# Kernel optimization log

Hardware: AMD Instinct MI355X
Metric: run time of the kernel (lower is better)

The kernel has to match this reference:

```python
import jax, jax.numpy as jnp
import numpy as np
import math

D_MODEL = 512
N_HEADS = 8
D_K = 64
BS = 16
SEQ = 512


def setup_inputs() -> dict:
    key = jax.random.key(0)
    ks = jax.random.split(key, 15)
    f = lambda k, sh, s=1.0: jax.random.normal(k, sh, dtype=jnp.float32) * s
    inp = {}
    for i, n in enumerate(["q_mean", "q_cov", "k_mean", "k_cov", "v_mean", "v_cov"]):
        inp[n] = f(ks[i], (BS, SEQ, D_MODEL))
    wscale = 1.0 / math.sqrt(D_MODEL)  # ~xavier
    for i, n in enumerate(["Wq_mean", "Wq_cov", "Wk_mean", "Wk_cov", "Wv_mean", "Wv_cov", "Wo_mean", "Wo_cov"]):
        inp[n] = f(ks[6 + i], (D_MODEL, D_MODEL), wscale)
    inp["gammas"] = f(ks[14], (N_HEADS, 1, 1), 0.5)  # xavier on (h,1,1)
    # causal mask: attend to positions j <= i
    inp["mask"] = jnp.tril(jnp.ones((SEQ, SEQ), dtype=jnp.int32))[None, None]
    return inp


def _heads(x, W):
    # torch Linear: x @ W.T ; bias is 0 by init. -> [bs, h, S, d_k]
    bs = x.shape[0]
    return (x @ W.T).reshape(bs, -1, N_HEADS, D_K).transpose(0, 2, 1, 3)


def _uattention(qm, qc, km, kc, vm, vc, mask, gammas):
    # Wasserstein-2 distance between diagonal Gaussians, fused into matmuls
    mean_d = (-2.0 * jnp.einsum('bhsd,bhtd->bhst', qm, km)
              + jnp.sum(qm ** 2, -1, keepdims=True)
              + jnp.sum(km ** 2, -1, keepdims=True).swapaxes(-1, -2))
    sqc = jnp.sqrt(jnp.clip(qc, 1e-24))
    skc = jnp.sqrt(jnp.clip(kc, 1e-24))
    cov_d = (-2.0 * jnp.einsum('bhsd,bhtd->bhst', sqc, skc)
             + jnp.sum(qc, -1, keepdims=True)
             + jnp.sum(kc, -1, keepdims=True).swapaxes(-1, -2))
    scores = -(mean_d + cov_d) / math.sqrt(D_K)  # [bs,h,S,S]

    maskb = (mask == 0)
    maskf = mask.astype(scores.dtype)

    def _dist(s):
        s_ = jax.nn.softmax(jnp.where(maskb, -1e32, s), axis=-1) * maskf
        cum = jnp.cumsum(s_, axis=-1)
        tot = jnp.sum(s_, axis=-1, keepdims=True)
        idx = jnp.arange(SEQ)
        pos = jnp.abs(idx[None, :] - idx[:, None]).astype(jnp.float32)[None, None]
        return jnp.sqrt(jnp.clip((tot - cum) * pos, 0.0))

    dist_scores = jax.lax.stop_gradient(_dist(scores))  # torch: no_grad + detach
    gamma = -jax.nn.softplus(gammas)[None]  # [1,h,1,1]
    total_effect = jnp.clip(jnp.exp(dist_scores * gamma), 1e-5, 1e5)
    scores = jnp.where(maskb, -1e32, scores * total_effect)
    scores = jax.nn.softmax(scores, axis=-1)
    scores = scores.at[:, :, 0, :].set(0.0)  # zero_pad
    out_mean = jnp.einsum('bhst,bhtd->bhsd', scores, vm)
    out_cov = jnp.einsum('bhst,bhtd->bhsd', scores ** 2, vc)
    return out_mean, out_cov


def reference(q_mean, q_cov, k_mean, k_cov, v_mean, v_cov,
              Wq_mean, Wq_cov, Wk_mean, Wk_cov, Wv_mean, Wv_cov,
              Wo_mean, Wo_cov, gammas, mask):
    bs = q_mean.shape[0]
    qm = _heads(q_mean, Wq_mean)
    qc = _heads(q_cov, Wq_cov)
    km = _heads(k_mean, Wk_mean)
    kc = _heads(k_cov, Wk_cov)
    vm = _heads(v_mean, Wv_mean)
    vc = _heads(v_cov, Wv_cov)
    om, oc = _uattention(qm, qc, km, kc, vm, vc, mask, gammas)
    cm = om.transpose(0, 2, 1, 3).reshape(bs, -1, D_MODEL)
    cc = oc.transpose(0, 2, 1, 3).reshape(bs, -1, D_MODEL)
    return cm @ Wo_mean.T, cc @ Wo_cov.T
```

## Files before the change

### kernel.cpp

```cpp
#include <hip/hip_runtime.h>
#include <hip/hip_bf16.h>

#define SEQ    512
#define DMODEL 512
#define NHEAD  8
#define DK     64
#define BS     16
#define NBH    (BS*NHEAD)
#define HSZ    (SEQ*DK)

typedef __attribute__((ext_vector_type(8))) short bf16x8;
typedef __attribute__((ext_vector_type(4))) float f32x4;

#define MFMA32(A,B,C) __builtin_amdgcn_mfma_f32_16x16x32_bf16(A,B,C,0,0,0)

#define WS_GAM 16ull
#define WS_AQM 256ull
#define WS_AQC (WS_AQM +  65536ull)
#define WS_BKM (WS_AQM + 131072ull)
#define WS_BKC (WS_AQM + 196608ull)
#define WS_AQF (WS_AQM + 262144ull)
#define WS_BKF (WS_AQM + 327680ull)
#define WS_OM  1048576ull
#define WS_OC  (WS_OM + 4194304ull)
#define WS_BF  (WS_OC + 4194304ull)
#define ARRE   4194304ull
#define A_QMH 0
#define A_QML 1
#define A_SCH 2
#define A_SCL 3
#define A_KMH 4
#define A_SKH 6
#define A_VMT 8
#define A_VCT 9

__device__ __forceinline__ unsigned short* warr(float* wsf, int idx) {
  return (unsigned short*)(wsf + WS_BF) + (size_t)idx * ARRE;
}

__device__ __forceinline__ float bf2f(unsigned short h) {
  union { float f; unsigned u; } v; v.u = ((unsigned)h) << 16; return v.f;
}
__device__ __forceinline__ unsigned short f2bf(float f) {
  union { float f; unsigned u; } v; v.f = f;
  unsigned u = v.u;
  u += 0x7FFFu + ((u >> 16) & 1u);
  return (unsigned short)(u >> 16);
}
__device__ __forceinline__ void ld8_f32(const float* p, float* v) {
  float4 a = *(const float4*)p; float4 b = *(const float4*)(p+4);
  v[0]=a.x;v[1]=a.y;v[2]=a.z;v[3]=a.w;v[4]=b.x;v[5]=b.y;v[6]=b.z;v[7]=b.w;
}
__device__ __forceinline__ unsigned pk2bf(float a, float b) {
  union { float f; unsigned u; } x, y;
  x.f = a; y.f = b;
  return __builtin_amdgcn_perm(y.u + 0x8000u, x.u + 0x8000u, 0x07060302u);
}
__device__ __forceinline__ uint4 cvt8r(const float* t8) {
  uint4 h;
  h.x = pk2bf(t8[0], t8[1]);
  h.y = pk2bf(t8[2], t8[3]);
  h.z = pk2bf(t8[4], t8[5]);
  h.w = pk2bf(t8[6], t8[7]);
  return h;
}
__device__ __forceinline__ uint4 cvt8h(const float* p) {
  float t8[8]; ld8_f32(p, t8); return cvt8r(t8);
}

__global__ void k_gamma(const float* __restrict__ g_in, float* __restrict__ wsf) {
  int t = threadIdx.x;
  if (t >= NHEAD) return;
  float g = g_in[t];
  float sp = (g > 20.f) ? g : log1pf(expf(g));
  (wsf + WS_GAM)[t] = -sp;
}

__global__ __launch_bounds__(256) void k_projM(
    const float* xqm, const float* xqc, const float* xkm, const float* xkc,
    const float* xvm, const float* xvc,
    const float* wqm, const float* wqc, const float* wkm, const float* wkc,
    const float* wvm, const float* wvc,
    float* wsf)
{
  __shared__ __align__(16) unsigned short Ah[4096];
  __shared__ __align__(16) unsigned short Bh[4096];
  const int y = blockIdx.y;
  const float* X; const float* W;
  unsigned short *outh = nullptr, *outl = nullptr;
  float* sums = nullptr;
  float qscale = 1.0f; int mode = 0;
  switch (y) {
    case 0: X=xqm; W=wqm; outh=warr(wsf,A_QMH); outl=warr(wsf,A_QML); sums=wsf+WS_AQM; qscale=0.25f; mode=0; break;
    case 1: X=xkm; W=wkm; outh=warr(wsf,A_KMH); outl=nullptr;         sums=wsf+WS_BKM; qscale=1.0f;  mode=0; break;
    case 2: X=xqc; W=wqc; outh=warr(wsf,A_SCH); outl=warr(wsf,A_SCL); sums=wsf+WS_AQC; qscale=0.25f; mode=1; break;
    case 3: X=xkc; W=wkc; outh=warr(wsf,A_SKH); outl=nullptr;         sums=wsf+WS_BKC; qscale=1.0f;  mode=1; break;
    case 4: X=xvm; W=wvm; outh=warr(wsf,A_VMT); mode=2; break;
    default:X=xvc; W=wvc; outh=warr(wsf,A_VCT); mode=2; break;
  }
  const int tid = threadIdx.x;
  const int l = tid & 63, li = l & 15, lg = l >> 4;
  const int w = tid >> 6, wr = w >> 1, wc = w & 1;
  const int blk = blockIdx.x;
  const int xcd = blk & 7, qq = blk >> 3;
  const int m0 = (xcd*8 + (qq & 7)) * 128;
  const int n0 = (qq >> 3) * 128;
  const int r0 = tid >> 2, c0 = tid & 3, r1 = r0 + 64;
  const int wo0 = r0*64 + ((c0 ^ ((r0>>1)&3))*16);
  const int wo1 = r1*64 + ((c0 ^ ((r1>>1)&3))*16);
  int roA[4], roB[4];
#pragma unroll
  for (int mi = 0; mi < 4; ++mi) {
    int r  = wr*64 + mi*16 + li;
    roA[mi] = r*64 + ((lg ^ ((r>>1)&3))*16);
    int rn = wc*64 + mi*16 + li;
    roB[mi] = rn*64 + ((lg ^ ((rn>>1)&3))*16);
  }
  const float* xp0 = X + (size_t)(m0+r0)*DMODEL + c0*8;
  const float* xp1 = X + (size_t)(m0+r1)*DMODEL + c0*8;
  const float* wp0 = W + (size_t)(n0+r0)*DMODEL + c0*8;
  const float* wp1 = W + (size_t)(n0+r1)*DMODEL + c0*8;
  uint4 a0 = cvt8h(xp0);
  uint4 a1 = cvt8h(xp1);
  uint4 b0 = cvt8h(wp0);
  uint4 b1 = cvt8h(wp1);

  f32x4 acc[4][4];
  f32x4 z = {0.f,0.f,0.f,0.f};
#pragma unroll
  for (int a = 0; a < 4; ++a)
#pragma unroll
    for (int b = 0; b < 4; ++b) acc[a][b] = z;

  for (int kt = 0; kt < DMODEL; kt += 32) {
    __syncthreads();
    *(uint4*)((char*)Ah + wo0) = a0;
    *(uint4*)((char*)Ah + wo1) = a1;
    *(uint4*)((char*)Bh + wo0) = b0;
    *(uint4*)((char*)Bh + wo1) = b1;
    __syncthreads();
    if (kt + 32 < DMODEL) {
      a0 = cvt8h(xp0 + kt + 32);
      a1 = cvt8h(xp1 + kt + 32);
      b0 = cvt8h(wp0 + kt + 32);
      b1 = cvt8h(wp1 + kt + 32);
    }
    bf16x8 ah[4], bh[4];
#pragma unroll
    for (int mi = 0; mi < 4; ++mi) {
      ah[mi] = *(const bf16x8*)((const char*)Ah + roA[mi]);
      bh[mi] = *(const bf16x8*)((const char*)Bh + roB[mi]);
    }
#pragma unroll
    for (int mi = 0; mi < 4; ++mi)
#pragma unroll
      for (int nj = 0; nj < 4; ++nj)
        acc[mi][nj] = MFMA32(ah[mi], bh[nj], acc[mi][nj]);
  }

  const int head = ((n0 >> 6) + wc);
  if (mode <= 1) {
    const bool kside = (outl == nullptr);
#pragma unroll
    for (int mi = 0; mi < 4; ++mi)
#pragma unroll
      for (int reg = 0; reg < 4; ++reg) {
        float rs = 0.f;
#pragma unroll
        for (int nj = 0; nj < 4; ++nj) {
          float v = acc[mi][nj][reg];
          if (mode == 0) {
            float vs = (kside) ? bf2f(f2bf(v)) : v;
            rs += vs*vs;
          } else {
            rs += v;
          }
        }
        rs += __shfl_xor(rs, 1); rs += __shfl_xor(rs, 2);
        rs += __shfl_xor(rs, 4); rs += __shfl_xor(rs, 8);
        if (li == 0) {
          int m = m0 + wr*64 + mi*16 + 4*lg + reg;
          sums[((size_t)(m >> 9)*NHEAD + head)*SEQ + (m & 511)] = rs;
        }
      }
#pragma unroll
    for (int mi = 0; mi < 4; ++mi)
#pragma unroll
      for (int nj = 0; nj < 4; ++nj)
#pragma unroll
        for (int reg = 0; reg < 4; ++reg) {
          float v = acc[mi][nj][reg];
          if (mode == 1) v = sqrtf(fmaxf(v, 1e-24f));
          v *= qscale;
          unsigned short h16 = f2bf(v);
          int m = m0 + wr*64 + mi*16 + 4*lg + reg;
          int n = n0 + wc*64 + nj*16 + li;
          size_t dst = ((size_t)((m >> 9)*NHEAD + (n >> 6))*SEQ + (m & 511))*DK + (n & 63);
          outh[dst] = h16;
          if (outl) outl[dst] = f2bf(v - bf2f(h16));
        }
  } else {
#pragma unroll
    for (int mi = 0; mi < 4; ++mi)
#pragma unroll
      for (int nj = 0; nj < 4; ++nj) {
        int mb = m0 + wr*64 + mi*16 + 4*lg;
        int n = n0 + wc*64 + nj*16 + li;
        int b = mb >> 9, s = mb & 511, d = n & 63;
        unsigned e0 = f2bf(acc[mi][nj][0]);
        unsigned e1 = f2bf(acc[mi][nj][1]);
        unsigned e2 = f2bf(acc[mi][nj][2]);
        unsigned e3 = f2bf(acc[mi][nj][3]);
        uint2 pk; pk.x = e0 | (e1 << 16); pk.y = e2 | (e3 << 16);
        *(uint2*)(outh + ((size_t)(b*NHEAD + head)*DK + d)*SEQ + s) = pk;
      }
  }
}

__global__ void k_sumAB(float* wsf) {
  int i = blockIdx.x * 256 + threadIdx.x;
  if (i < NBH*SEQ) {
    (wsf+WS_AQF)[i] = 0.125f * ((wsf+WS_AQM)[i] + (wsf+WS_AQC)[i]);
    (wsf+WS_BKF)[i] = 0.125f * ((wsf+WS_BKM)[i] + (wsf+WS_BKC)[i]);
  }
}

__global__ __launch_bounds__(128) void k_attn2(float* wsf)
{
  __shared__ float s_bk[SEQ];
  __shared__ float s_ex[2][2][16];
  __shared__ __align__(16) float s_acc[64][33];

  const unsigned short* qmh = warr(wsf, A_QMH);
  const unsigned short* qml = warr(wsf, A_QML);
  const unsigned short* sch = warr(wsf, A_SCH);
  const unsigned short* scl = warr(wsf, A_SCL);
  const unsigned short* kmh = warr(wsf, A_KMH);
  const unsigned short* skh = warr(wsf, A_SKH);
  const unsigned short* vmT = warr(wsf, A_VMT);
  const unsigned short* vcT = warr(wsf, A_VCT);
  float* omF = wsf + WS_OM;
  float* ocF = wsf + WS_OC;
  const float* AqF = wsf + WS_AQF;
  const float* BkF = wsf + WS_BKF;

  const int tid = threadIdx.x;
  const int l = tid & 63, li = l & 15, lg = l >> 4;
  const int w = tid >> 6;
  const int blk = blockIdx.x;
  const int xcd = blk & 7;
  const int q   = blk >> 3;
  const int bh  = xcd*16 + (q & 15);
  const int rt  = 31 - (q >> 4);
  const int i = rt*16 + li;
  const int ntile = rt + 1;
  const int h0 = (ntile + 1) >> 1;
  const int tstart = w ? h0 : 0;
  const int tend   = w ? ntile : h0;
  const float gam = (wsf + WS_GAM)[bh & (NHEAD-1)];
  const float aq = AqF[(size_t)bh*SEQ + i];

  for (int idx = tid; idx < SEQ; idx += 128) s_bk[idx] = BkF[(size_t)bh*SEQ + idx];

  bf16x8 qf[8];
  {
    const unsigned short* qb[4] = {qmh, qml, sch, scl};
#pragma unroll
    for (int part = 0; part < 2; ++part)
#pragma unroll
      for (int hl = 0; hl < 2; ++hl)
#pragma unroll
        for (int ks = 0; ks < 2; ++ks)
          qf[part*4 + ks*2 + hl] =
            *(const bf16x8*)(qb[part*2+hl] + ((size_t)bh*SEQ + i)*DK + ks*32 + lg*8);
  }
  __syncthreads();

  auto score_tile = [&](int t, float* s) {
    const int j0 = t*16;
    f32x4 accA = {0.f,0.f,0.f,0.f};
    f32x4 accB = {0.f,0.f,0.f,0.f};
    const size_t krow = ((size_t)bh*SEQ + j0 + li)*DK + lg*8;
#pragma unroll
    for (int part = 0; part < 2; ++part) {
      const unsigned short* khp = part ? skh : kmh;
#pragma unroll
      for (int ks = 0; ks < 2; ++ks) {
        bf16x8 kh = *(const bf16x8*)(khp + krow + ks*32);
        accA = MFMA32(kh, qf[part*4+ks*2+0], accA);
        accB = MFMA32(kh, qf[part*4+ks*2+1], accB);
      }
    }
    const float4 bk4 = *(const float4*)&s_bk[j0 + lg*4];
    float bks[4] = {bk4.x, bk4.y, bk4.z, bk4.w};
#pragma unroll
    for (int r = 0; r < 4; ++r) {
      int j = j0 + lg*4 + r;
      float v = (accA[r] + accB[r]) - aq - bks[r];
      s[r] = (j > i) ? -3.0e38f : v;
    }
  };

  float m1 = -3.0e38f, tot = 0.f;
  for (int t = tstart; t < tend; ++t) {
    float s[4]; score_tile(t, s);
    float tm = fmaxf(fmaxf(s[0], s[1]), fmaxf(s[2], s[3]));
    tm = fmaxf(tm, __shfl_xor(tm, 16));
    tm = fmaxf(tm, __shfl_xor(tm, 32));
    float m1n = fmaxf(m1, tm);
    float lsum = __expf(s[0]-m1n) + __expf(s[1]-m1n) + __expf(s[2]-m1n) + __expf(s[3]-m1n);
    lsum += __shfl_xor(lsum, 16); lsum += __shfl_xor(lsum, 32);
    tot = tot * __expf(m1 - m1n) + lsum;
    m1 = m1n;
  }
  if (lg == 0) { s_ex[w][0][li] = m1; s_ex[w][1][li] = tot; }
  __syncthreads();
  float run;
  {
    float m0 = s_ex[0][0][li], t0 = s_ex[0][1][li];
    float m1b = s_ex[1][0][li], t1 = s_ex[1][1][li];
    float mg = fmaxf(m0, m1b);
    float e0 = __expf(m0 - mg), e1 = __expf(m1b - mg);
    tot = t0*e0 + t1*e1;
    run = w ? t0*e0 : 0.f;
    m1 = mg;
  }
  const float invtot = 1.0f / tot;

  f32x4 accm[4], accc[4];
  {
    f32x4 z = {0.f,0.f,0.f,0.f};
#pragma unroll
    for (int dt = 0; dt < 4; ++dt) { accm[dt] = z; accc[dt] = z; }
  }
  float m2 = -3.0e38f, sum2 = 0.f;

  auto scan_tile = [&](int t, float* s2) {
    float s[4]; score_tile(t, s);
    float e0 = __expf(s[0]-m1), e1 = __expf(s[1]-m1),
          e2 = __expf(s[2]-m1), e3 = __expf(s[3]-m1);
    float p0 = e0, p1 = p0+e1, p2 = p1+e2, p3 = p2+e3;
    float lt = p3;
    float a = __shfl_up(lt, 16), b = __shfl_up(lt, 32), c = __shfl_up(lt, 48);
    float excl = (lg >= 1 ? a : 0.f) + (lg >= 2 ? b : 0.f) + (lg >= 3 ? c : 0.f);
    float base = run + excl;
    float cums[4] = {base+p0, base+p1, base+p2, base+p3};
    float ttr = lt;
    ttr += __shfl_xor(ttr, 16); ttr += __shfl_xor(ttr, 32);
    run += ttr;
#pragma unroll
    for (int r = 0; r < 4; ++r) {
      int j = t*16 + lg*4 + r;
      float rem = fmaxf(tot - cums[r], 0.f) * invtot;
      float pos = fmaxf((float)(i - j), 0.f);
      float dist = sqrtf(rem * pos);
      float eff = fmaxf(__expf(dist * gam), 1e-5f);
      s2[r] = (j > i) ? -3.0e38f : s[r] * eff;
    }
  };

  for (int t0 = tstart; t0 < tend; t0 += 2) {
    float s2A[4], s2B[4];
    scan_tile(t0, s2A);
    const bool hasB = (t0 + 1) < tend;
    if (hasB) scan_tile(t0+1, s2B);
    else { s2B[0]=s2B[1]=s2B[2]=s2B[3] = -3.0e38f; }
    float mt = fmaxf(fmaxf(fmaxf(s2A[0],s2A[1]), fmaxf(s2A[2],s2A[3])),
                     fmaxf(fmaxf(s2B[0],s2B[1]), fmaxf(s2B[2],s2B[3])));
    mt = fmaxf(mt, __shfl_xor(mt, 16));
    mt = fmaxf(mt, __shfl_xor(mt, 32));
    float m2n = fmaxf(m2, mt);
    float scale = __expf(m2 - m2n);
    float scale2 = scale * scale;
#pragma unroll
    for (int dt = 0; dt < 4; ++dt) { accm[dt] *= scale; accc[dt] *= scale2; }
    float pA[4], pB[4];
#pragma unroll
    for (int r = 0; r < 4; ++r) { pA[r] = __expf(s2A[r]-m2n); pB[r] = __expf(s2B[r]-m2n); }
    float ps = pA[0]+pA[1]+pA[2]+pA[3] + pB[0]+pB[1]+pB[2]+pB[3];
    ps += __shfl_xor(ps, 16); ps += __shfl_xor(ps, 32);
    sum2 = sum2 * scale + ps;
    m2 = m2n;
    union PU { uint4 u; bf16x8 v; } pm, pc;
    pm.u.x = pk2bf(pA[0], pA[1]); pm.u.y = pk2bf(pA[2], pA[3]);
    pm.u.z = pk2bf(pB[0], pB[1]); pm.u.w = pk2bf(pB[2], pB[3]);
    pc.u.x = pk2bf(pA[0]*pA[0], pA[1]*pA[1]); pc.u.y = pk2bf(pA[2]*pA[2], pA[3]*pA[3]);
    pc.u.z = pk2bf(pB[0]*pB[0], pB[1]*pB[1]); pc.u.w = pk2bf(pB[2]*pB[2], pB[3]*pB[3]);
    const int j0A = t0*16;
    const int j0B = hasB ? j0A + 16 : j0A;
    union V16 { struct { uint2 lo, hi; } u; bf16x8 v; };
#pragma unroll
    for (int dt = 0; dt < 4; ++dt) {
      const size_t vrow = ((size_t)bh*DK + dt*16 + li)*SEQ;
      V16 vm_, vc_;
      vm_.u.lo = *(const uint2*)(vmT + vrow + j0A + lg*4);
      vm_.u.hi = *(const uint2*)(vmT + vrow + j0B + lg*4);
      vc_.u.lo = *(const uint2*)(vcT + vrow + j0A + lg*4);
      vc_.u.hi = *(const uint2*)(vcT + vrow + j0B + lg*4);
      accm[dt] = MFMA32(vm_.v, pm.v, accm[dt]);
      accc[dt] = MFMA32(vc_.v, pc.v, accc[dt]);
    }
  }

  __syncthreads();
  if (lg == 0) s_ex[w][0][li] = m2;
  __syncthreads();
  const float m2g = fmaxf(s_ex[0][0][li], s_ex[1][0][li]);
  const float sc = __expf(m2 - m2g);
  const float sc2 = sc * sc;
  if (w == 1) {
#pragma unroll
    for (int dt = 0; dt < 4; ++dt)
#pragma unroll
      for (int reg = 0; reg < 4; ++reg) {
        s_acc[l][dt*4 + reg]      = accm[dt][reg] * sc;
        s_acc[l][16 + dt*4 + reg] = accc[dt][reg] * sc2;
      }
    if (lg == 0) s_ex[1][1][li] = sum2 * sc;
  }
  __syncthreads();
  if (w == 0) {
    const float sum2g = sum2 * sc + s_ex[1][1][li];
    const float inv2 = 1.0f / sum2g;
    const float inv2c = inv2 * inv2;
    const bool zero = (i == 0);
    float* om_p = omF + ((size_t)bh*SEQ + i)*DK;
    float* oc_p = ocF + ((size_t)bh*SEQ + i)*DK;
#pragma unroll
    for (int dt = 0; dt < 4; ++dt) {
      float4 vm4, vc4;
      vm4.x = (accm[dt][0]*sc + s_acc[l][dt*4+0]) * inv2;
      vm4.y = (accm[dt][1]*sc + s_acc[l][dt*4+1]) * inv2;
      vm4.z = (accm[dt][2]*sc + s_acc[l][dt*4+2]) * inv2;
      vm4.w = (accm[dt][3]*sc + s_acc[l][dt*4+3]) * inv2;
      vc4.x = (accc[dt][0]*sc2 + s_acc[l][16+dt*4+0]) * inv2c;
      vc4.y = (accc[dt][1]*sc2 + s_acc[l][16+dt*4+1]) * inv2c;
      vc4.z = (accc[dt][2]*sc2 + s_acc[l][16+dt*4+2]) * inv2c;
      vc4.w = (accc[dt][3]*sc2 + s_acc[l][16+dt*4+3]) * inv2c;
      if (zero) { vm4 = make_float4(0.f,0.f,0.f,0.f); vc4 = vm4; }
      *(float4*)(om_p + dt*16 + lg*4) = vm4;
      *(float4*)(oc_p + dt*16 + lg*4) = vc4;
    }
  }
}

__global__ __launch_bounds__(256) void k_outM(float* wsf,
                                              const float* w_mean, const float* w_cov,
                                              float* outp)
{
  __shared__ __align__(16) unsigned short Ah[4096];
  __shared__ __align__(16) unsigned short Bh[4096];
  const int y = blockIdx.y;
  const float* A = wsf + (y ? WS_OC : WS_OM);
  const float* W = y ? w_cov : w_mean;
  float* out = outp + (size_t)y * 4194304ull;

  const int tid = threadIdx.x;
  const int l = tid & 63, li = l & 15, lg = l >> 4;
  const int w = tid >> 6, wr = w >> 1, wc = w & 1;
  const int blk = blockIdx.x;
  const int xcd = blk & 7, qq = blk >> 3;
  const int m0 = (xcd*8 + (qq & 7)) * 128;
  const int n0 = (qq >> 3) * 128;
  const int r0 = tid >> 2, c0 = tid & 3, r1 = r0 + 64;
  const int wo0 = r0*64 + ((c0 ^ ((r0>>1)&3))*16);
  const int wo1 = r1*64 + ((c0 ^ ((r1>>1)&3))*16);
  int roA[4], roB[4];
#pragma unroll
  for (int mi = 0; mi < 4; ++mi) {
    int r  = wr*64 + mi*16 + li;
    roA[mi] = r*64 + ((lg ^ ((r>>1)&3))*16);
    int rn = wc*64 + mi*16 + li;
    roB[mi] = rn*64 + ((lg ^ ((rn>>1)&3))*16);
  }
  const int mA0 = m0 + r0, mA1 = m0 + r1;
  const size_t abase0 = ((size_t)(mA0 >> 9) * NHEAD * SEQ + (mA0 & 511)) * DK;
  const size_t abase1 = ((size_t)(mA1 >> 9) * NHEAD * SEQ + (mA1 & 511)) * DK;
  const float* wp0 = W + (size_t)(n0 + r0)*DMODEL + c0*8;
  const float* wp1 = W + (size_t)(n0 + r1)*DMODEL + c0*8;

  auto acvt = [&](size_t abase, int k) -> uint4 {
    const float* p = A + abase + (size_t)(k >> 6) * (SEQ*DK) + (k & 63);
    return cvt8h(p);
  };

  int k0 = c0*8;
  uint4 a0 = acvt(abase0, k0);
  uint4 a1 = acvt(abase1, k0);
  uint4 b0 = cvt8h(wp0);
  uint4 b1 = cvt8h(wp1);

  f32x4 acc[4][4];
  f32x4 z = {0.f,0.f,0.f,0.f};
#pragma unroll
  for (int a = 0; a < 4; ++a)
#pragma unroll
    for (int b = 0; b < 4; ++b) acc[a][b] = z;

  for (int kt = 0; kt < DMODEL; kt += 32) {
    __syncthreads();
    *(uint4*)((char*)Ah + wo0) = a0;
    *(uint4*)((char*)Ah + wo1) = a1;
    *(uint4*)((char*)Bh + wo0) = b0;
    *(uint4*)((char*)Bh + wo1) = b1;
    __syncthreads();
    if (kt + 32 < DMODEL) {
      int kn = kt + 32 + c0*8;
      a0 = acvt(abase0, kn);
      a1 = acvt(abase1, kn);
      b0 = cvt8h(wp0 + kt + 32);
      b1 = cvt8h(wp1 + kt + 32);
    }
    bf16x8 ah[4], bh[4];
#pragma unroll
    for (int mi = 0; mi < 4; ++mi) {
      ah[mi] = *(const bf16x8*)((const char*)Ah + roA[mi]);
      bh[mi] = *(const bf16x8*)((const char*)Bh + roB[mi]);
    }
#pragma unroll
    for (int mi = 0; mi < 4; ++mi)
#pragma unroll
      for (int nj = 0; nj < 4; ++nj)
        acc[mi][nj] = MFMA32(ah[mi], bh[nj], acc[mi][nj]);
  }
#pragma unroll
  for (int mi = 0; mi < 4; ++mi)
#pragma unroll
    for (int nj = 0; nj < 4; ++nj)
#pragma unroll
      for (int reg = 0; reg < 4; ++reg) {
        int m = m0 + wr*64 + mi*16 + 4*lg + reg;
        int n = n0 + wc*64 + nj*16 + li;
        out[(size_t)m*DMODEL + n] = acc[mi][nj][reg];
      }
}

extern "C" void kernel_launch(void* const* d_in, const int* in_sizes, int n_in,
                              void* d_out, int out_size, void* d_ws, size_t ws_size,
                              hipStream_t stream) {
  (void)in_sizes; (void)n_in; (void)out_size; (void)ws_size;
  float* wsf = (float*)d_ws;

  k_gamma<<<1, 64, 0, stream>>>((const float*)d_in[14], wsf);
  k_projM<<<dim3(256, 6), 256, 0, stream>>>(
      (const float*)d_in[0], (const float*)d_in[1],
      (const float*)d_in[2], (const float*)d_in[3],
      (const float*)d_in[4], (const float*)d_in[5],
      (const float*)d_in[6], (const float*)d_in[7],
      (const float*)d_in[8], (const float*)d_in[9],
      (const float*)d_in[10], (const float*)d_in[11],
      wsf);
  k_sumAB<<<256, 256, 0, stream>>>(wsf);
  k_attn2<<<4096, 128, 0, stream>>>(wsf);
  k_outM<<<dim3(256, 2), 256, 0, stream>>>(wsf, (const float*)d_in[12],
                                           (const float*)d_in[13], (float*)d_out);
}
```

Measured before the change: 243.6 us.

## Split attention key range across four waves and use exp2 with prescaled scores

Each attention block now uses four waves instead of two. Each wave takes a quarter of the causal key tiles, and the partial softmax statistics and accumulators are merged through shared memory. Scores and gamma are prescaled by log2(e) so exp2 can replace expf, and the V tile loads are hoisted ahead of the softmax math to hide latency. This shortens the per-block serial chain at the cost of more shared memory, an extra merge step, and higher register pressure.

```diff
diff --git a/kernel.cpp b/kernel.cpp
--- a/kernel.cpp
+++ b/kernel.cpp
@@ -8,6 +8,7 @@
 #define BS     16
 #define NBH    (BS*NHEAD)
 #define HSZ    (SEQ*DK)
+#define L2E    1.4426950408889634f
 
 typedef __attribute__((ext_vector_type(8))) short bf16x8;
 typedef __attribute__((ext_vector_type(4))) float f32x4;
@@ -73,7 +74,7 @@
   if (t >= NHEAD) return;
   float g = g_in[t];
   float sp = (g > 20.f) ? g : log1pf(expf(g));
-  (wsf + WS_GAM)[t] = -sp;
+  (wsf + WS_GAM)[t] = -sp * L2E;
 }
 
 __global__ __launch_bounds__(256) void k_projM(
@@ -91,10 +92,10 @@
   float* sums = nullptr;
   float qscale = 1.0f; int mode = 0;
   switch (y) {
-    case 0: X=xqm; W=wqm; outh=warr(wsf,A_QMH); outl=warr(wsf,A_QML); sums=wsf+WS_AQM; qscale=0.25f; mode=0; break;
-    case 1: X=xkm; W=wkm; outh=warr(wsf,A_KMH); outl=nullptr;         sums=wsf+WS_BKM; qscale=1.0f;  mode=0; break;
-    case 2: X=xqc; W=wqc; outh=warr(wsf,A_SCH); outl=warr(wsf,A_SCL); sums=wsf+WS_AQC; qscale=0.25f; mode=1; break;
-    case 3: X=xkc; W=wkc; outh=warr(wsf,A_SKH); outl=nullptr;         sums=wsf+WS_BKC; qscale=1.0f;  mode=1; break;
+    case 0: X=xqm; W=wqm; outh=warr(wsf,A_QMH); outl=warr(wsf,A_QML); sums=wsf+WS_AQM; qscale=0.25f*L2E; mode=0; break;
+    case 1: X=xkm; W=wkm; outh=warr(wsf,A_KMH); outl=nullptr;         sums=wsf+WS_BKM; qscale=1.0f;      mode=0; break;
+    case 2: X=xqc; W=wqc; outh=warr(wsf,A_SCH); outl=warr(wsf,A_SCL); sums=wsf+WS_AQC; qscale=0.25f*L2E; mode=1; break;
+    case 3: X=xkc; W=wkc; outh=warr(wsf,A_SKH); outl=nullptr;         sums=wsf+WS_BKC; qscale=1.0f;      mode=1; break;
     case 4: X=xvm; W=wvm; outh=warr(wsf,A_VMT); mode=2; break;
     default:X=xvc; W=wvc; outh=warr(wsf,A_VCT); mode=2; break;
   }
@@ -220,16 +221,16 @@
 __global__ void k_sumAB(float* wsf) {
   int i = blockIdx.x * 256 + threadIdx.x;
   if (i < NBH*SEQ) {
-    (wsf+WS_AQF)[i] = 0.125f * ((wsf+WS_AQM)[i] + (wsf+WS_AQC)[i]);
-    (wsf+WS_BKF)[i] = 0.125f * ((wsf+WS_BKM)[i] + (wsf+WS_BKC)[i]);
-  }
-}
-
-__global__ __launch_bounds__(128) void k_attn2(float* wsf)
+    (wsf+WS_AQF)[i] = (0.125f*L2E) * ((wsf+WS_AQM)[i] + (wsf+WS_AQC)[i]);
+    (wsf+WS_BKF)[i] = (0.125f*L2E) * ((wsf+WS_BKM)[i] + (wsf+WS_BKC)[i]);
+  }
+}
+
+__global__ __launch_bounds__(256) void k_attn2(float* wsf)
 {
   __shared__ float s_bk[SEQ];
-  __shared__ float s_ex[2][2][16];
-  __shared__ __align__(16) float s_acc[64][33];
+  __shared__ float s_ex[4][2][16];
+  __shared__ __align__(16) float s_acc[3][64][33];
 
   const unsigned short* qmh = warr(wsf, A_QMH);
   const unsigned short* qml = warr(wsf, A_QML);
@@ -254,13 +255,13 @@
   const int rt  = 31 - (q >> 4);
   const int i = rt*16 + li;
   const int ntile = rt + 1;
-  const int h0 = (ntile + 1) >> 1;
-  const int tstart = w ? h0 : 0;
-  const int tend   = w ? ntile : h0;
+  const int qd = ntile >> 2, rr = ntile & 3;
+  const int tstart = w*qd + (w < rr ? w : rr);
+  const int tend   = tstart + qd + (w < rr ? 1 : 0);
   const float gam = (wsf + WS_GAM)[bh & (NHEAD-1)];
   const float aq = AqF[(size_t)bh*SEQ + i];
 
-  for (int idx = tid; idx < SEQ; idx += 128) s_bk[idx] = BkF[(size_t)bh*SEQ + idx];
+  for (int idx = tid; idx < SEQ; idx += 256) s_bk[idx] = BkF[(size_t)bh*SEQ + idx];
 
   bf16x8 qf[8];
   {
@@ -308,21 +309,24 @@
     tm = fmaxf(tm, __shfl_xor(tm, 16));
     tm = fmaxf(tm, __shfl_xor(tm, 32));
     float m1n = fmaxf(m1, tm);
-    float lsum = __expf(s[0]-m1n) + __expf(s[1]-m1n) + __expf(s[2]-m1n) + __expf(s[3]-m1n);
+    float lsum = exp2f(s[0]-m1n) + exp2f(s[1]-m1n) + exp2f(s[2]-m1n) + exp2f(s[3]-m1n);
     lsum += __shfl_xor(lsum, 16); lsum += __shfl_xor(lsum, 32);
-    tot = tot * __expf(m1 - m1n) + lsum;
+    tot = tot * exp2f(m1 - m1n) + lsum;
     m1 = m1n;
   }
   if (lg == 0) { s_ex[w][0][li] = m1; s_ex[w][1][li] = tot; }
   __syncthreads();
   float run;
   {
-    float m0 = s_ex[0][0][li], t0 = s_ex[0][1][li];
-    float m1b = s_ex[1][0][li], t1 = s_ex[1][1][li];
-    float mg = fmaxf(m0, m1b);
-    float e0 = __expf(m0 - mg), e1 = __expf(m1b - mg);
-    tot = t0*e0 + t1*e1;
-    run = w ? t0*e0 : 0.f;
+    float mA = s_ex[0][0][li], mB = s_ex[1][0][li],
+          mC = s_ex[2][0][li], mD = s_ex[3][0][li];
+    float mg = fmaxf(fmaxf(mA, mB), fmaxf(mC, mD));
+    float tA = s_ex[0][1][li] * exp2f(mA - mg);
+    float tB = s_ex[1][1][li] * exp2f(mB - mg);
+    float tC = s_ex[2][1][li] * exp2f(mC - mg);
+    float tD = s_ex[3][1][li] * exp2f(mD - mg);
+    tot = tA + tB + tC + tD;
+    run = (w > 0 ? tA : 0.f) + (w > 1 ? tB : 0.f) + (w > 2 ? tC : 0.f);
     m1 = mg;
   }
   const float invtot = 1.0f / tot;
@@ -337,8 +341,8 @@
 
   auto scan_tile = [&](int t, float* s2) {
     float s[4]; score_tile(t, s);
-    float e0 = __expf(s[0]-m1), e1 = __expf(s[1]-m1),
-          e2 = __expf(s[2]-m1), e3 = __expf(s[3]-m1);
+    float e0 = exp2f(s[0]-m1), e1 = exp2f(s[1]-m1),
+          e2 = exp2f(s[2]-m1), e3 = exp2f(s[3]-m1);
     float p0 = e0, p1 = p0+e1, p2 = p1+e2, p3 = p2+e3;
     float lt = p3;
     float a = __shfl_up(lt, 16), b = __shfl_up(lt, 32), c = __shfl_up(lt, 48);
@@ -354,7 +358,7 @@
       float rem = fmaxf(tot - cums[r], 0.f) * invtot;
       float pos = fmaxf((float)(i - j), 0.f);
       float dist = sqrtf(rem * pos);
-      float eff = fmaxf(__expf(dist * gam), 1e-5f);
+      float eff = fmaxf(exp2f(dist * gam), 1e-5f);
       s2[r] = (j > i) ? -3.0e38f : s[r] * eff;
     }
   };
@@ -365,18 +369,30 @@
     const bool hasB = (t0 + 1) < tend;
     if (hasB) scan_tile(t0+1, s2B);
     else { s2B[0]=s2B[1]=s2B[2]=s2B[3] = -3.0e38f; }
+    const int j0A = t0*16;
+    const int j0B = hasB ? j0A + 16 : j0A;
+    union V16 { struct { uint2 lo, hi; } u; bf16x8 v; };
+    V16 vm_[4], vc_[4];
+#pragma unroll
+    for (int dt = 0; dt < 4; ++dt) {
+      const size_t vrow = ((size_t)bh*DK + dt*16 + li)*SEQ;
+      vm_[dt].u.lo = *(const uint2*)(vmT + vrow + j0A + lg*4);
+      vm_[dt].u.hi = *(const uint2*)(vmT + vrow + j0B + lg*4);
+      vc_[dt].u.lo = *(const uint2*)(vcT + vrow + j0A + lg*4);
+      vc_[dt].u.hi = *(const uint2*)(vcT + vrow + j0B + lg*4);
+    }
     float mt = fmaxf(fmaxf(fmaxf(s2A[0],s2A[1]), fmaxf(s2A[2],s2A[3])),
                      fmaxf(fmaxf(s2B[0],s2B[1]), fmaxf(s2B[2],s2B[3])));
     mt = fmaxf(mt, __shfl_xor(mt, 16));
     mt = fmaxf(mt, __shfl_xor(mt, 32));
     float m2n = fmaxf(m2, mt);
-    float scale = __expf(m2 - m2n);
+    float scale = exp2f(m2 - m2n);
     float scale2 = scale * scale;
 #pragma unroll
     for (int dt = 0; dt < 4; ++dt) { accm[dt] *= scale; accc[dt] *= scale2; }
     float pA[4], pB[4];
 #pragma unroll
-    for (int r = 0; r < 4; ++r) { pA[r] = __expf(s2A[r]-m2n); pB[r] = __expf(s2B[r]-m2n); }
+    for (int r = 0; r < 4; ++r) { pA[r] = exp2f(s2A[r]-m2n); pB[r] = exp2f(s2B[r]-m2n); }
     float ps = pA[0]+pA[1]+pA[2]+pA[3] + pB[0]+pB[1]+pB[2]+pB[3];
     ps += __shfl_xor(ps, 16); ps += __shfl_xor(ps, 32);
     sum2 = sum2 * scale + ps;
@@ -386,41 +402,33 @@
     pm.u.z = pk2bf(pB[0], pB[1]); pm.u.w = pk2bf(pB[2], pB[3]);
     pc.u.x = pk2bf(pA[0]*pA[0], pA[1]*pA[1]); pc.u.y = pk2bf(pA[2]*pA[2], pA[3]*pA[3]);
     pc.u.z = pk2bf(pB[0]*pB[0], pB[1]*pB[1]); pc.u.w = pk2bf(pB[2]*pB[2], pB[3]*pB[3]);
-    const int j0A = t0*16;
-    const int j0B = hasB ? j0A + 16 : j0A;
-    union V16 { struct { uint2 lo, hi; } u; bf16x8 v; };
 #pragma unroll
     for (int dt = 0; dt < 4; ++dt) {
-      const size_t vrow = ((size_t)bh*DK + dt*16 + li)*SEQ;
-      V16 vm_, vc_;
-      vm_.u.lo = *(const uint2*)(vmT + vrow + j0A + lg*4);
-      vm_.u.hi = *(const uint2*)(vmT + vrow + j0B + lg*4);
-      vc_.u.lo = *(const uint2*)(vcT + vrow + j0A + lg*4);
-      vc_.u.hi = *(const uint2*)(vcT + vrow + j0B + lg*4);
-      accm[dt] = MFMA32(vm_.v, pm.v, accm[dt]);
-      accc[dt] = MFMA32(vc_.v, pc.v, accc[dt]);
+      accm[dt] = MFMA32(vm_[dt].v, pm.v, accm[dt]);
+      accc[dt] = MFMA32(vc_[dt].v, pc.v, accc[dt]);
     }
   }
 
   __syncthreads();
   if (lg == 0) s_ex[w][0][li] = m2;
   __syncthreads();
-  const float m2g = fmaxf(s_ex[0][0][li], s_ex[1][0][li]);
-  const float sc = __expf(m2 - m2g);
+  const float m2g = fmaxf(fmaxf(s_ex[0][0][li], s_ex[1][0][li]),
+                          fmaxf(s_ex[2][0][li], s_ex[3][0][li]));
+  const float sc = exp2f(m2 - m2g);
   const float sc2 = sc * sc;
-  if (w == 1) {
+  if (w > 0) {
 #pragma unroll
     for (int dt = 0; dt < 4; ++dt)
 #pragma unroll
       for (int reg = 0; reg < 4; ++reg) {
-        s_acc[l][dt*4 + reg]      = accm[dt][reg] * sc;
-        s_acc[l][16 + dt*4 + reg] = accc[dt][reg] * sc2;
+        s_acc[w-1][l][dt*4 + reg]      = accm[dt][reg] * sc;
+        s_acc[w-1][l][16 + dt*4 + reg] = accc[dt][reg] * sc2;
       }
-    if (lg == 0) s_ex[1][1][li] = sum2 * sc;
+    if (lg == 0) s_ex[w][1][li] = sum2 * sc;
   }
   __syncthreads();
   if (w == 0) {
-    const float sum2g = sum2 * sc + s_ex[1][1][li];
+    const float sum2g = sum2 * sc + s_ex[1][1][li] + s_ex[2][1][li] + s_ex[3][1][li];
     const float inv2 = 1.0f / sum2g;
     const float inv2c = inv2 * inv2;
     const bool zero = (i == 0);
@@ -429,14 +437,14 @@
 #pragma unroll
     for (int dt = 0; dt < 4; ++dt) {
       float4 vm4, vc4;
-      vm4.x = (accm[dt][0]*sc + s_acc[l][dt*4+0]) * inv2;
-      vm4.y = (accm[dt][1]*sc + s_acc[l][dt*4+1]) * inv2;
-      vm4.z = (accm[dt][2]*sc + s_acc[l][dt*4+2]) * inv2;
-      vm4.w = (accm[dt][3]*sc + s_acc[l][dt*4+3]) * inv2;
-      vc4.x = (accc[dt][0]*sc2 + s_acc[l][16+dt*4+0]) * inv2c;
-      vc4.y = (accc[dt][1]*sc2 + s_acc[l][16+dt*4+1]) * inv2c;
-      vc4.z = (accc[dt][2]*sc2 + s_acc[l][16+dt*4+2]) * inv2c;
-      vc4.w = (accc[dt][3]*sc2 + s_acc[l][16+dt*4+3]) * inv2c;
+      vm4.x = (accm[dt][0]*sc + s_acc[0][l][dt*4+0] + s_acc[1][l][dt*4+0] + s_acc[2][l][dt*4+0]) * inv2;
+      vm4.y = (accm[dt][1]*sc + s_acc[0][l][dt*4+1] + s_acc[1][l][dt*4+1] + s_acc[2][l][dt*4+1]) * inv2;
+      vm4.z = (accm[dt][2]*sc + s_acc[0][l][dt*4+2] + s_acc[1][l][dt*4+2] + s_acc[2][l][dt*4+2]) * inv2;
+      vm4.w = (accm[dt][3]*sc + s_acc[0][l][dt*4+3] + s_acc[1][l][dt*4+3] + s_acc[2][l][dt*4+3]) * inv2;
+      vc4.x = (accc[dt][0]*sc2 + s_acc[0][l][16+dt*4+0] + s_acc[1][l][16+dt*4+0] + s_acc[2][l][16+dt*4+0]) * inv2c;
+      vc4.y = (accc[dt][1]*sc2 + s_acc[0][l][16+dt*4+1] + s_acc[1][l][16+dt*4+1] + s_acc[2][l][16+dt*4+1]) * inv2c;
+      vc4.z = (accc[dt][2]*sc2 + s_acc[0][l][16+dt*4+2] + s_acc[1][l][16+dt*4+2] + s_acc[2][l][16+dt*4+2]) * inv2c;
+      vc4.w = (accc[dt][3]*sc2 + s_acc[0][l][16+dt*4+3] + s_acc[1][l][16+dt*4+3] + s_acc[2][l][16+dt*4+3]) * inv2c;
       if (zero) { vm4 = make_float4(0.f,0.f,0.f,0.f); vc4 = vm4; }
       *(float4*)(om_p + dt*16 + lg*4) = vm4;
       *(float4*)(oc_p + dt*16 + lg*4) = vc4;
@@ -551,7 +559,7 @@
       (const float*)d_in[10], (const float*)d_in[11],
       wsf);
   k_sumAB<<<256, 256, 0, stream>>>(wsf);
-  k_attn2<<<4096, 128, 0, stream>>>(wsf);
+  k_attn2<<<4096, 256, 0, stream>>>(wsf);
   k_outM<<<dim3(256, 2), 256, 0, stream>>>(wsf, (const float*)d_in[12],
                                            (const float*)d_in[13], (float*)d_out);
 }
```

New measurement: 268.1 us (median of 2 runs). 1.1x slower.
